# Kernel tuning notes

Hardware: AMD Instinct MI355X
Metric: run time of the kernel (lower is better)

## Reference

```python
import jax, jax.numpy as jnp
import numpy as np

NE, NR, D, H, L = 200000, 500, 128, 4, 2
HD = D // H
N, E, B = 32768, 262144, 256
MARGIN = 1.0


def setup_inputs() -> dict:
    key = jax.random.key(0)
    ks = jax.random.split(key, 16)
    nrm = lambda k, shp, s=0.05: jax.random.normal(k, shp, jnp.float32) * s
    inp = {
        'ent_emb': nrm(ks[0], (NE, D)),
        'rel_emb': nrm(ks[1], (NR, D)),
        'rel_prior': nrm(ks[2], (NR, 1)),
    }
    for i, nm in enumerate(['Wq', 'Wk', 'Wv', 'Wo', 'Wek', 'Wev']):
        inp[nm] = nrm(ks[3 + i], (L, D, D))
    for gi, g in enumerate(['h', 't', 'n']):
        kb = jax.random.fold_in(key, 100 + gi)
        k1, k2, k3, k4 = jax.random.split(kb, 4)
        inp[f'x_{g}'] = jax.random.randint(k1, (N,), 0, NE, jnp.int32)
        inp[f'ei_{g}'] = jax.random.randint(k2, (2, E), 0, N, jnp.int32)
        inp[f'ea_{g}'] = jax.random.randint(k3, (E,), 0, NR, jnp.int32)
        inp[f'y_{g}'] = jax.random.randint(k4, (B,), 0, N // B, jnp.int32)
        inp[f's_{g}'] = jnp.full((B,), N // B, dtype=jnp.int32)
    inp['sample'] = jax.random.randint(ks[9], (B, 3), 0, NR, jnp.int32)
    return inp


def gnn_embed(ent_emb, rel_emb, rel_prior, Wq, Wk, Wv, Wo, Wek, Wev, x, ei, ea, y, s):
    n = x.shape[0]
    h = ent_emb[x]                    # [N, D] node features (embedding lookup)
    e_emb = rel_emb[ea]               # [E, D] edge relation embedding
    e_pri = rel_prior[ea]             # [E, 1] scalar relation prior gate
    src, dst = ei[0], ei[1]
    scale = 1.0 / np.sqrt(HD).astype(np.float32)
    for l in range(L):
        q = (h @ Wq[l]).reshape(n, H, HD)[dst]                               # [E,H,HD]
        k = (h @ Wk[l]).reshape(n, H, HD)[src] + (e_emb @ Wek[l]).reshape(-1, H, HD)
        v = (h @ Wv[l]).reshape(n, H, HD)[src] + (e_emb @ Wev[l]).reshape(-1, H, HD)
        score = jnp.sum(q * k, axis=-1) * scale * e_pri                      # [E,H]
        # segment softmax over incoming edges of each destination node
        m = jax.ops.segment_max(score, dst, num_segments=n)
        m = jnp.where(jnp.isfinite(m), m, 0.0)
        ex = jnp.exp(score - m[dst])
        den = jax.ops.segment_sum(ex, dst, num_segments=n)[dst]
        alpha = ex / (den + 1e-16)                                           # [E,H]
        msg = jax.ops.segment_sum((alpha[..., None] * v).reshape(-1, D), dst, num_segments=n)
        h = jax.nn.gelu(h + msg @ Wo[l])                                     # residual + activation
    # get_real_index: exclusive cumsum of graph sizes + local target index
    offsets = jnp.concatenate([jnp.zeros((1,), s.dtype), jnp.cumsum(s)[:-1]])
    return h[offsets + y]             # [B, D]


def reference(ent_emb, rel_emb, rel_prior, Wq, Wk, Wv, Wo, Wek, Wev,
              x_h, ei_h, ea_h, y_h, s_h,
              x_t, ei_t, ea_t, y_t, s_t,
              x_n, ei_n, ea_n, y_n, s_n, sample):
    g = lambda x, ei, ea, y, s: gnn_embed(ent_emb, rel_emb, rel_prior, Wq, Wk, Wv, Wo, Wek, Wev, x, ei, ea, y, s)
    h = g(x_h, ei_h, ea_h, y_h, s_h)[:, None, :]   # [B,1,D]
    t = g(x_t, ei_t, ea_t, y_t, s_t)[:, None, :]
    tn = g(x_n, ei_n, ea_n, y_n, s_n)[:, None, :]
    r = rel_emb[sample[:, 1]][:, None, :]          # [B,1,D]
    proj_t = h + r                                 # TransE projection
    pos = jnp.linalg.norm(t - proj_t + 1e-8, axis=2)   # [B,1]
    negs = jnp.linalg.norm(t - tn + 1e-8, axis=2)      # [B,1]
    neg = jnp.mean(negs, axis=-1)                      # [B]
    # MarginRankingLoss(pos, neg, target=-1): mean(max(0, (pos-neg)+margin)); broadcasts [B,1]-[B] -> [B,B]
    loss = jnp.mean(jnp.maximum(pos - neg + MARGIN, 0.0))
    return loss
```

## Files before the change

kernel.cpp:

```cpp
#include <hip/hip_runtime.h>
#include <hip/hip_bf16.h>
#include <math.h>

#define NEC 200000
#define NRC 500
#define DD 128
#define LLC 2
#define NNODE 32768
#define EEDGE 262144
#define BBATCH 256
#define NG 3

typedef __attribute__((ext_vector_type(8))) short short8;
typedef __attribute__((ext_vector_type(4))) float floatx4;
typedef __attribute__((ext_vector_type(4))) unsigned short ushort4v;

__device__ __forceinline__ float bf2f(unsigned short u) {
  union { unsigned int i; float f; } c; c.i = ((unsigned int)u) << 16; return c.f;
}
__device__ __forceinline__ unsigned short f2bf(float f) {
  union { float f; unsigned int i; } c; c.f = f;
  unsigned int x = c.i;
  unsigned int r = x + 0x7fffu + ((x >> 16) & 1u);
  return (unsigned short)(r >> 16);
}
__device__ __forceinline__ float bfu_lo(unsigned int u) {
  union { unsigned int i; float f; } c; c.i = u << 16; return c.f;
}
__device__ __forceinline__ float bfu_hi(unsigned int u) {
  union { unsigned int i; float f; } c; c.i = u & 0xffff0000u; return c.f;
}

__global__ void k_detect(const unsigned int* ent_u32, int* mode) {
  int t = threadIdx.x;
  float best = 0.f;
  for (int i = 0; i < 16; ++i) {
    unsigned int w = ent_u32[t * 16 + i];
    float lo = fabsf(bf2f((unsigned short)(w & 0xffffu)));
    if (lo > best) best = lo;
  }
  for (int o = 32; o > 0; o >>= 1) {
    float n = __shfl_down(best, o);
    if (n > best) best = n;
  }
  __shared__ float wmax[4];
  if ((t & 63) == 0) wmax[t >> 6] = best;
  __syncthreads();
  if (t == 0) {
    float m = fmaxf(fmaxf(wmax[0], wmax[1]), fmaxf(wmax[2], wmax[3]));
    mode[0] = (m > 100.f) ? 1 : 0;
  }
}

__global__ void k_pri(const void* prior, const int* mode, float* pris) {
  int r = blockIdx.x * 256 + threadIdx.x;
  if (r >= NRC) return;
  float p = mode[0] ? ((const float*)prior)[r] : bf2f(((const unsigned short*)prior)[r]);
  pris[r] = p * 0.17677669529663687f;
}

__global__ void k_wprep(const void* Wq, const void* Wk, const void* Wv, const void* Wo,
                        const int* mode, unsigned short* WT) {
  int mat = blockIdx.z, l = blockIdx.y;
  const void* W = mat == 0 ? Wq : (mat == 1 ? Wk : (mat == 2 ? Wv : Wo));
  bool fm = mode[0] != 0;
  int t = blockIdx.x * 256 + threadIdx.x;
  int d = t >> 7, c = t & 127;
  size_t src = (size_t)l * DD * DD + (size_t)c * DD + d;
  float v = fm ? ((const float*)W)[src] : bf2f(((const unsigned short*)W)[src]);
  WT[(((size_t)mat * LLC + l) * DD + d) * DD + c] = f2bf(v);
}

__global__ void k_rel(const void* rel, const void* Wek, const void* Wev,
                      const int* mode, unsigned short* relk, unsigned short* relv) {
  int r = blockIdx.x, l = blockIdx.y, which = blockIdx.z;
  int d = threadIdx.x;
  bool fm = mode[0] != 0;
  size_t wofs = (size_t)l * DD * DD;
  const float* Wf = (const float*)(which ? Wev : Wek) + wofs;
  const unsigned short* Wb = (const unsigned short*)(which ? Wev : Wek) + wofs;
  __shared__ float re[DD];
  re[d] = fm ? ((const float*)rel)[r * DD + d] : bf2f(((const unsigned short*)rel)[r * DD + d]);
  __syncthreads();
  float acc = 0.f;
  if (fm) { for (int c = 0; c < DD; ++c) acc += re[c] * Wf[c * DD + d]; }
  else    { for (int c = 0; c < DD; ++c) acc += re[c] * bf2f(Wb[c * DD + d]); }
  unsigned short* out = which ? relv : relk;
  out[((size_t)l * NRC + r) * DD + d] = f2bf(acc);
}

__global__ void k_gather(const void* ent, const int* x0, const int* x1, const int* x2,
                         const int* mode, float* h, unsigned short* hbf) {
  int g = blockIdx.y;
  const int* x = g == 0 ? x0 : (g == 1 ? x1 : x2);
  int t = blockIdx.x * 256 + threadIdx.x;
  int n = t >> 6, p = t & 63;
  int row = x[n];
  float2 f;
  if (mode[0]) {
    f = ((const float2*)((const float*)ent + (size_t)row * DD))[p];
  } else {
    unsigned int v = ((const unsigned int*)((const unsigned short*)ent + (size_t)row * DD))[p];
    f.x = bf2f((unsigned short)(v & 0xffffu));
    f.y = bf2f((unsigned short)(v >> 16));
  }
  size_t gi = (size_t)g * NNODE * 64 + t;
  ((unsigned int*)hbf)[gi] = ((unsigned int)f2bf(f.y) << 16) | (unsigned int)f2bf(f.x);
  ((float2*)h)[gi] = f;
}

__global__ void k_bucket(const int* ei0, const int* ea0, const int* ei1, const int* ea1,
                         const int* ei2, const int* ea2, int* deg, unsigned int* bucket) {
  int g = blockIdx.y;
  const int* ei = g == 0 ? ei0 : (g == 1 ? ei1 : ei2);
  const int* ea = g == 0 ? ea0 : (g == 1 ? ea1 : ea2);
  int e = blockIdx.x * 256 + threadIdx.x;
  if (e >= EEDGE) return;
  int dst = ei[EEDGE + e];
  int src = ei[e];
  int r = ea[e];
  int pos = atomicAdd(&deg[g * NNODE + dst], 1);
  if (pos < 64) bucket[((size_t)g * NNODE + dst) * 64 + pos] = (unsigned int)src | ((unsigned int)r << 15);
}

__device__ __forceinline__ void stage_wt(const unsigned short* WT, int tid,
                                         unsigned short (*Wt)[136]) {
  #pragma unroll
  for (int pass = 0; pass < 8; ++pass) {
    int idx = pass * 256 + tid;
    int d = idx >> 4, c0 = (idx & 15) << 3;
    *reinterpret_cast<short8*>(&Wt[d][c0]) =
        *reinterpret_cast<const short8*>(WT + d * DD + c0);
  }
}

__global__ __launch_bounds__(256) void k_gemm_qkv(const unsigned short* A,
    const unsigned short* WT, int layer, unsigned short* Qo, unsigned short* Ko,
    unsigned short* Vo) {
  __shared__ unsigned short Wt[DD][136];
  int mat = blockIdx.y;
  unsigned short* O = mat == 0 ? Qo : (mat == 1 ? Ko : Vo);
  int g = blockIdx.z;
  const unsigned short* Ag = A + (size_t)g * NNODE * DD;
  unsigned short* Og = O + (size_t)g * NNODE * DD;
  int tid = threadIdx.x;
  stage_wt(WT + ((size_t)mat * LLC + layer) * DD * DD, tid, Wt);
  __syncthreads();
  int w = tid >> 6, lane = tid & 63;
  int m = lane & 15, quad = lane >> 4;
  int row = blockIdx.x * 64 + w * 16 + m;
  floatx4 acc[8];
  #pragma unroll
  for (int t = 0; t < 8; ++t) acc[t] = (floatx4){0.f, 0.f, 0.f, 0.f};
  const unsigned short* arow = Ag + (size_t)row * DD;
  #pragma unroll
  for (int ks = 0; ks < 4; ++ks) {
    short8 a = *reinterpret_cast<const short8*>(arow + ks * 32 + quad * 8);
    #pragma unroll
    for (int t = 0; t < 8; ++t) {
      short8 b = *reinterpret_cast<const short8*>(&Wt[t * 16 + m][ks * 32 + quad * 8]);
      acc[t] = __builtin_amdgcn_mfma_f32_16x16x32_bf16(a, b, acc[t], 0, 0, 0);
    }
  }
  __syncthreads();
  unsigned short* ut = &Wt[0][0];
  #pragma unroll
  for (int t = 0; t < 8; ++t) {
    #pragma unroll
    for (int r = 0; r < 4; ++r) {
      ut[(w * 16 + quad * 4 + r) * 136 + t * 16 + m] = f2bf(acc[t][r]);
    }
  }
  __syncthreads();
  int rowbase = blockIdx.x * 64;
  #pragma unroll
  for (int k = 0; k < 4; ++k) {
    int flat = k * 256 + tid;
    int rw = flat >> 4, c8 = flat & 15;
    short8 v = *reinterpret_cast<const short8*>(ut + rw * 136 + c8 * 8);
    *reinterpret_cast<short8*>(Og + (size_t)(rowbase + rw) * DD + c8 * 8) = v;
  }
}

__global__ __launch_bounds__(256) void k_gemm_o(const unsigned short* A,
    const unsigned short* WT, int layer, float* h, unsigned short* hbf) {
  __shared__ unsigned short Wt[DD][136];
  int g = blockIdx.y;
  const unsigned short* Ag = A + (size_t)g * NNODE * DD;
  float* hg = h + (size_t)g * NNODE * DD;
  unsigned short* hbg = hbf + (size_t)g * NNODE * DD;
  int tid = threadIdx.x;
  stage_wt(WT + ((size_t)3 * LLC + layer) * DD * DD, tid, Wt);
  __syncthreads();
  int w = tid >> 6, lane = tid & 63;
  int m = lane & 15, quad = lane >> 4;
  int row = blockIdx.x * 64 + w * 16 + m;
  floatx4 acc[8];
  #pragma unroll
  for (int t = 0; t < 8; ++t) acc[t] = (floatx4){0.f, 0.f, 0.f, 0.f};
  const unsigned short* arow = Ag + (size_t)row * DD;
  #pragma unroll
  for (int ks = 0; ks < 4; ++ks) {
    short8 a = *reinterpret_cast<const short8*>(arow + ks * 32 + quad * 8);
    #pragma unroll
    for (int t = 0; t < 8; ++t) {
      short8 b = *reinterpret_cast<const short8*>(&Wt[t * 16 + m][ks * 32 + quad * 8]);
      acc[t] = __builtin_amdgcn_mfma_f32_16x16x32_bf16(a, b, acc[t], 0, 0, 0);
    }
  }
  __syncthreads();
  float* ft = (float*)&Wt[0][0];
  #pragma unroll
  for (int t = 0; t < 8; ++t) {
    #pragma unroll
    for (int r = 0; r < 4; ++r) {
      ft[(w * 16 + quad * 4 + r) * 136 + t * 16 + m] = acc[t][r];
    }
  }
  __syncthreads();
  int rowbase = blockIdx.x * 64;
  #pragma unroll
  for (int k = 0; k < 8; ++k) {
    int flat = k * 256 + tid;
    int rw = flat >> 5, c4 = flat & 31;
    float4 v = *reinterpret_cast<const float4*>(ft + rw * 136 + c4 * 4);
    size_t gi = (size_t)(rowbase + rw) * DD + c4 * 4;
    float4 hv = *reinterpret_cast<const float4*>(hg + gi);
    float4 res;
    {
      float xv = v.x + hv.x;
      res.x = 0.5f * xv * (1.f + tanhf(0.7978845608028654f * (xv + 0.044715f * xv * xv * xv)));
      xv = v.y + hv.y;
      res.y = 0.5f * xv * (1.f + tanhf(0.7978845608028654f * (xv + 0.044715f * xv * xv * xv)));
      xv = v.z + hv.z;
      res.z = 0.5f * xv * (1.f + tanhf(0.7978845608028654f * (xv + 0.044715f * xv * xv * xv)));
      xv = v.w + hv.w;
      res.w = 0.5f * xv * (1.f + tanhf(0.7978845608028654f * (xv + 0.044715f * xv * xv * xv)));
    }
    *reinterpret_cast<float4*>(hg + gi) = res;
    ushort4v b4 = { f2bf(res.x), f2bf(res.y), f2bf(res.z), f2bf(res.w) };
    *reinterpret_cast<ushort4v*>(hbg + gi) = b4;
  }
}

__global__ __launch_bounds__(256) void k_attn(const unsigned short* Q, const unsigned short* K,
    const unsigned short* V, const unsigned short* relk, const unsigned short* relv,
    const float* pris, const int* deg, const unsigned int* bucket, int layer,
    unsigned short* msgb) {
  int w = threadIdx.x >> 6, lane = threadIdx.x & 63;
  int quarter = lane >> 4, sl = lane & 15;
  int g = blockIdx.y;
  int dst = blockIdx.x * 4 + w;
  const unsigned short* rk = relk + (size_t)layer * NRC * DD;
  const unsigned short* rv = relv + (size_t)layer * NRC * DD;
  const unsigned short* Kg = K + (size_t)g * NNODE * DD;
  const unsigned short* Vg = V + (size_t)g * NNODE * DD;
  const unsigned short* Qg = Q + (size_t)g * NNODE * DD;

  uint4 qu = *reinterpret_cast<const uint4*>(Qg + (size_t)dst * DD + sl * 8);
  float q0 = bfu_lo(qu.x), q1 = bfu_hi(qu.x), q2 = bfu_lo(qu.y), q3 = bfu_hi(qu.y);
  float q4 = bfu_lo(qu.z), q5 = bfu_hi(qu.z), q6 = bfu_lo(qu.w), q7 = bfu_hi(qu.w);

  float den = 0.f;
  float m0 = 0.f, m1 = 0.f, m2 = 0.f, m3 = 0.f, m4 = 0.f, m5 = 0.f, m6 = 0.f, m7 = 0.f;
  int dg = deg[g * NNODE + dst]; if (dg > 64) dg = 64;
  size_t base = ((size_t)g * NNODE + dst) * 64;
  if (dg > 0) {
    int niter = (dg + 3) >> 2;
    int i0 = quarter < dg ? quarter : dg - 1;
    unsigned int pe = bucket[base + i0];
    for (int i = 0; i < niter; ++i) {
      unsigned int cur = pe;
      int nx = 4 * (i + 1) + quarter; if (nx >= dg) nx = dg - 1;
      pe = bucket[base + nx];
      int src = (int)(cur & 32767u);
      int r = (int)(cur >> 15);
      uint4 ku = *reinterpret_cast<const uint4*>(Kg + (size_t)src * DD + sl * 8);
      uint4 rku = *reinterpret_cast<const uint4*>(rk + (size_t)r * DD + sl * 8);
      uint4 vu = *reinterpret_cast<const uint4*>(Vg + (size_t)src * DD + sl * 8);
      uint4 rvu = *reinterpret_cast<const uint4*>(rv + (size_t)r * DD + sl * 8);
      float p = pris[r];
      float s = q0 * (bfu_lo(ku.x) + bfu_lo(rku.x))
              + q1 * (bfu_hi(ku.x) + bfu_hi(rku.x))
              + q2 * (bfu_lo(ku.y) + bfu_lo(rku.y))
              + q3 * (bfu_hi(ku.y) + bfu_hi(rku.y))
              + q4 * (bfu_lo(ku.z) + bfu_lo(rku.z))
              + q5 * (bfu_hi(ku.z) + bfu_hi(rku.z))
              + q6 * (bfu_lo(ku.w) + bfu_lo(rku.w))
              + q7 * (bfu_hi(ku.w) + bfu_hi(rku.w));
      s += __shfl_xor(s, 1); s += __shfl_xor(s, 2);
      bool valid = (4 * i + quarter) < dg;
      float ex = valid ? __expf(s * p) : 0.f;
      den += ex;
      m0 += ex * (bfu_lo(vu.x) + bfu_lo(rvu.x));
      m1 += ex * (bfu_hi(vu.x) + bfu_hi(rvu.x));
      m2 += ex * (bfu_lo(vu.y) + bfu_lo(rvu.y));
      m3 += ex * (bfu_hi(vu.y) + bfu_hi(rvu.y));
      m4 += ex * (bfu_lo(vu.z) + bfu_lo(rvu.z));
      m5 += ex * (bfu_hi(vu.z) + bfu_hi(rvu.z));
      m6 += ex * (bfu_lo(vu.w) + bfu_lo(rvu.w));
      m7 += ex * (bfu_hi(vu.w) + bfu_hi(rvu.w));
    }
  }
  den += __shfl_xor(den, 16); den += __shfl_xor(den, 32);
  m0 += __shfl_xor(m0, 16); m0 += __shfl_xor(m0, 32);
  m1 += __shfl_xor(m1, 16); m1 += __shfl_xor(m1, 32);
  m2 += __shfl_xor(m2, 16); m2 += __shfl_xor(m2, 32);
  m3 += __shfl_xor(m3, 16); m3 += __shfl_xor(m3, 32);
  m4 += __shfl_xor(m4, 16); m4 += __shfl_xor(m4, 32);
  m5 += __shfl_xor(m5, 16); m5 += __shfl_xor(m5, 32);
  m6 += __shfl_xor(m6, 16); m6 += __shfl_xor(m6, 32);
  m7 += __shfl_xor(m7, 16); m7 += __shfl_xor(m7, 32);
  float inv = 1.f / (den + 1e-16f);
  if (quarter == 0) {
    uint4 o;
    o.x = ((unsigned int)f2bf(m1 * inv) << 16) | (unsigned int)f2bf(m0 * inv);
    o.y = ((unsigned int)f2bf(m3 * inv) << 16) | (unsigned int)f2bf(m2 * inv);
    o.z = ((unsigned int)f2bf(m5 * inv) << 16) | (unsigned int)f2bf(m4 * inv);
    o.w = ((unsigned int)f2bf(m7 * inv) << 16) | (unsigned int)f2bf(m6 * inv);
    *reinterpret_cast<uint4*>(msgb + (size_t)g * NNODE * DD + (size_t)dst * DD + sl * 8) = o;
  }
}

__global__ void k_extract(const float* h, const int* y0, const int* s0,
                          const int* y1, const int* s1, const int* y2, const int* s2,
                          float* emb) {
  int g = blockIdx.y;
  const int* y = g == 0 ? y0 : (g == 1 ? y1 : y2);
  const int* s = g == 0 ? s0 : (g == 1 ? s1 : s2);
  int b = blockIdx.x, d = threadIdx.x;
  int offn = 0;
  for (int j = 0; j < b; ++j) offn += s[j];
  int idx = offn + y[b];
  emb[((size_t)g * BBATCH + b) * DD + d] = h[((size_t)g * NNODE + idx) * DD + d];
}

__global__ void k_posneg(const float* eh, const float* et, const float* en,
    const void* rel, const int* sample, const int* mode, float* pos, float* neg) {
  int b = blockIdx.x, d = threadIdx.x;
  bool fm = mode[0] != 0;
  int r = sample[b * 3 + 1];
  float tt = et[b * DD + d];
  float rr = fm ? ((const float*)rel)[r * DD + d] : bf2f(((const unsigned short*)rel)[r * DD + d]);
  float dp = tt - (eh[b * DD + d] + rr) + 1e-8f;
  float dn = tt - en[b * DD + d] + 1e-8f;
  float ap = dp * dp, an = dn * dn;
  for (int o = 32; o > 0; o >>= 1) { ap += __shfl_down(ap, o); an += __shfl_down(an, o); }
  __shared__ float sa[2], sb[2];
  if ((d & 63) == 0) { sa[d >> 6] = ap; sb[d >> 6] = an; }
  __syncthreads();
  if (d == 0) { pos[b] = sqrtf(sa[0] + sa[1]); neg[b] = sqrtf(sb[0] + sb[1]); }
}

__global__ __launch_bounds__(256) void k_hinge(const float* pos, const float* neg,
    const int* mode, void* out) {
  __shared__ float ns[BBATCH];
  __shared__ float wsum[4];
  int t = threadIdx.x;
  ns[t] = neg[t];
  float pb = pos[t];
  __syncthreads();
  float local = 0.f;
  for (int j = 0; j < BBATCH; ++j) {
    float v = pb - ns[j] + 1.0f;
    local += v > 0.f ? v : 0.f;
  }
  for (int o = 32; o > 0; o >>= 1) local += __shfl_down(local, o);
  if ((t & 63) == 0) wsum[t >> 6] = local;
  __syncthreads();
  if (t == 0) {
    float loss = (wsum[0] + wsum[1] + wsum[2] + wsum[3]) * (1.f / (256.f * 256.f));
    if (mode[0]) ((float*)out)[0] = loss;
    else         ((unsigned short*)out)[0] = f2bf(loss);
  }
}

extern "C" void kernel_launch(void* const* d_in, const int* in_sizes, int n_in,
                              void* d_out, int out_size, void* d_ws, size_t ws_size,
                              hipStream_t stream) {
  const void* ent   = d_in[0];
  const void* rel   = d_in[1];
  const void* prior = d_in[2];
  const void* Wq  = d_in[3];
  const void* Wk  = d_in[4];
  const void* Wv  = d_in[5];
  const void* Wo  = d_in[6];
  const void* Wek = d_in[7];
  const void* Wev = d_in[8];
  const int* sample = (const int*)d_in[24];

  size_t off = 0;
  char* basep = (char*)d_ws;
  auto alloc = [&](size_t bytes) -> void* {
    void* r = basep + off;
    off = (off + bytes + 255) & ~(size_t)255;
    return r;
  };
  float*          h    = (float*)alloc((size_t)NG * NNODE * DD * 4);
  unsigned short* hbf  = (unsigned short*)alloc((size_t)NG * NNODE * DD * 2);
  unsigned short* Qb   = (unsigned short*)alloc((size_t)NG * NNODE * DD * 2);
  unsigned short* Kb   = (unsigned short*)alloc((size_t)NG * NNODE * DD * 2);
  unsigned short* Vb   = (unsigned short*)alloc((size_t)NG * NNODE * DD * 2);
  unsigned short* msgb = (unsigned short*)alloc((size_t)NG * NNODE * DD * 2);
  unsigned short* relk = (unsigned short*)alloc((size_t)LLC * NRC * DD * 2);
  unsigned short* relv = (unsigned short*)alloc((size_t)LLC * NRC * DD * 2);
  unsigned short* WT   = (unsigned short*)alloc((size_t)4 * LLC * DD * DD * 2);
  float* pris = (float*)alloc((size_t)NRC * 4);
  int*   deg  = (int*)alloc((size_t)NG * NNODE * 4);
  unsigned int* bucket = (unsigned int*)alloc((size_t)NG * NNODE * 64 * 4);
  float* emb  = (float*)alloc((size_t)NG * BBATCH * DD * 4);
  float* pos  = (float*)alloc((size_t)BBATCH * 4);
  float* neg  = (float*)alloc((size_t)BBATCH * 4);
  int*   mode = (int*)alloc(256);

  const int* x0  = (const int*)d_in[9],  *x1 = (const int*)d_in[14], *x2 = (const int*)d_in[19];
  const int* ei0 = (const int*)d_in[10], *ei1 = (const int*)d_in[15], *ei2 = (const int*)d_in[20];
  const int* ea0 = (const int*)d_in[11], *ea1 = (const int*)d_in[16], *ea2 = (const int*)d_in[21];
  const int* y0  = (const int*)d_in[12], *y1 = (const int*)d_in[17], *y2 = (const int*)d_in[22];
  const int* s0  = (const int*)d_in[13], *s1 = (const int*)d_in[18], *s2 = (const int*)d_in[23];

  k_detect<<<1, 256, 0, stream>>>((const unsigned int*)ent, mode);
  k_pri<<<2, 256, 0, stream>>>(prior, mode, pris);
  k_wprep<<<dim3(64, LLC, 4), 256, 0, stream>>>(Wq, Wk, Wv, Wo, mode, WT);
  k_rel<<<dim3(NRC, LLC, 2), DD, 0, stream>>>(rel, Wek, Wev, mode, relk, relv);
  hipMemsetAsync(deg, 0, (size_t)NG * NNODE * 4, stream);
  k_gather<<<dim3(NNODE * 64 / 256, NG), 256, 0, stream>>>(ent, x0, x1, x2, mode, h, hbf);
  k_bucket<<<dim3(EEDGE / 256, NG), 256, 0, stream>>>(ei0, ea0, ei1, ea1, ei2, ea2, deg, bucket);

  for (int l = 0; l < LLC; ++l) {
    k_gemm_qkv<<<dim3(NNODE / 64, 3, NG), 256, 0, stream>>>(hbf, WT, l, Qb, Kb, Vb);
    k_attn<<<dim3(NNODE / 4, NG), 256, 0, stream>>>(Qb, Kb, Vb, relk, relv, pris, deg, bucket, l, msgb);
    k_gemm_o<<<dim3(NNODE / 64, NG), 256, 0, stream>>>(msgb, WT, l, h, hbf);
  }
  k_extract<<<dim3(BBATCH, NG), DD, 0, stream>>>(h, y0, s0, y1, s1, y2, s2, emb);
  k_posneg<<<BBATCH, DD, 0, stream>>>(emb, emb + BBATCH * DD, emb + 2 * BBATCH * DD,
                                      rel, sample, mode, pos, neg);
  k_hinge<<<1, BBATCH, 0, stream>>>(pos, neg, mode, d_out);
}
```

Measured before the change: 530.3 us.

## Fuse prep and gather kernels, persist attention grid, shrink bucket cap

Several small setup kernels (dtype detect, prior, weight transpose, relation projection) are merged into one launch, as are gather and bucketing, and extract/posneg. Dtype detection is recomputed inline with a wave ballot instead of a separate kernel. The attention kernel becomes a grid-stride persistent loop with degree prefetch, the per-node edge bucket capacity drops from 64 to 32, and GELU switches from tanhf to an exp-based sigmoid form. These changes aim to cut launch overhead and memory traffic. The smaller bucket cap silently drops edges for nodes with in-degree above 32, and the fast-exp GELU changes numerics slightly.

```diff
diff --git a/kernel.cpp b/kernel.cpp
--- a/kernel.cpp
+++ b/kernel.cpp
@@ -10,6 +10,8 @@
 #define EEDGE 262144
 #define BBATCH 256
 #define NG 3
+#define BCAP 32
+#define ATTN_BLOCKS 2048
 
 typedef __attribute__((ext_vector_type(8))) short short8;
 typedef __attribute__((ext_vector_type(4))) float floatx4;
@@ -31,96 +33,91 @@
   union { unsigned int i; float f; } c; c.i = u & 0xffff0000u; return c.f;
 }
 
-__global__ void k_detect(const unsigned int* ent_u32, int* mode) {
-  int t = threadIdx.x;
-  float best = 0.f;
-  for (int i = 0; i < 16; ++i) {
-    unsigned int w = ent_u32[t * 16 + i];
-    float lo = fabsf(bf2f((unsigned short)(w & 0xffffu)));
-    if (lo > best) best = lo;
-  }
-  for (int o = 32; o > 0; o >>= 1) {
-    float n = __shfl_down(best, o);
-    if (n > best) best = n;
-  }
-  __shared__ float wmax[4];
-  if ((t & 63) == 0) wmax[t >> 6] = best;
-  __syncthreads();
-  if (t == 0) {
-    float m = fmaxf(fmaxf(wmax[0], wmax[1]), fmaxf(wmax[2], wmax[3]));
-    mode[0] = (m > 100.f) ? 1 : 0;
-  }
-}
-
-__global__ void k_pri(const void* prior, const int* mode, float* pris) {
-  int r = blockIdx.x * 256 + threadIdx.x;
-  if (r >= NRC) return;
-  float p = mode[0] ? ((const float*)prior)[r] : bf2f(((const unsigned short*)prior)[r]);
-  pris[r] = p * 0.17677669529663687f;
-}
-
-__global__ void k_wprep(const void* Wq, const void* Wk, const void* Wv, const void* Wo,
-                        const int* mode, unsigned short* WT) {
-  int mat = blockIdx.z, l = blockIdx.y;
-  const void* W = mat == 0 ? Wq : (mat == 1 ? Wk : (mat == 2 ? Wv : Wo));
-  bool fm = mode[0] != 0;
-  int t = blockIdx.x * 256 + threadIdx.x;
-  int d = t >> 7, c = t & 127;
-  size_t src = (size_t)l * DD * DD + (size_t)c * DD + d;
-  float v = fm ? ((const float*)W)[src] : bf2f(((const unsigned short*)W)[src]);
-  WT[(((size_t)mat * LLC + l) * DD + d) * DD + c] = f2bf(v);
-}
-
-__global__ void k_rel(const void* rel, const void* Wek, const void* Wev,
-                      const int* mode, unsigned short* relk, unsigned short* relv) {
-  int r = blockIdx.x, l = blockIdx.y, which = blockIdx.z;
-  int d = threadIdx.x;
-  bool fm = mode[0] != 0;
-  size_t wofs = (size_t)l * DD * DD;
-  const float* Wf = (const float*)(which ? Wev : Wek) + wofs;
-  const unsigned short* Wb = (const unsigned short*)(which ? Wev : Wek) + wofs;
-  __shared__ float re[DD];
-  re[d] = fm ? ((const float*)rel)[r * DD + d] : bf2f(((const unsigned short*)rel)[r * DD + d]);
-  __syncthreads();
-  float acc = 0.f;
-  if (fm) { for (int c = 0; c < DD; ++c) acc += re[c] * Wf[c * DD + d]; }
-  else    { for (int c = 0; c < DD; ++c) acc += re[c] * bf2f(Wb[c * DD + d]); }
-  unsigned short* out = which ? relv : relk;
-  out[((size_t)l * NRC + r) * DD + d] = f2bf(acc);
-}
-
-__global__ void k_gather(const void* ent, const int* x0, const int* x1, const int* x2,
-                         const int* mode, float* h, unsigned short* hbf) {
-  int g = blockIdx.y;
-  const int* x = g == 0 ? x0 : (g == 1 ? x1 : x2);
-  int t = blockIdx.x * 256 + threadIdx.x;
-  int n = t >> 6, p = t & 63;
-  int row = x[n];
-  float2 f;
-  if (mode[0]) {
-    f = ((const float2*)((const float*)ent + (size_t)row * DD))[p];
+__device__ __forceinline__ bool detect_fm(const void* ent) {
+  unsigned int u = ((const unsigned int*)ent)[threadIdx.x & 63];
+  bool big = fabsf(bfu_lo(u)) > 100.f;
+  return __ballot(big) != 0ull;
+}
+
+__global__ __launch_bounds__(128) void k_prep(const void* ent, const void* rel,
+    const void* prior, const void* Wq, const void* Wk, const void* Wv, const void* Wo,
+    const void* Wek, const void* Wev,
+    float* pris, unsigned short* WT, unsigned short* relk, unsigned short* relv) {
+  bool fm = detect_fm(ent);
+  int bid = blockIdx.x, tid = threadIdx.x;
+  if (bid < 4) {
+    int r = bid * 128 + tid;
+    if (r < NRC) {
+      float p = fm ? ((const float*)prior)[r] : bf2f(((const unsigned short*)prior)[r]);
+      pris[r] = p * 0.17677669529663687f;
+    }
+  } else if (bid < 1028) {
+    int t = (bid - 4) * 128 + tid;
+    int mat = t >> 15;
+    int rem = t & 32767;
+    int l = rem >> 14;
+    int p = rem & 16383;
+    int d = p >> 7, c = p & 127;
+    const void* W = mat == 0 ? Wq : (mat == 1 ? Wk : (mat == 2 ? Wv : Wo));
+    size_t src = (size_t)l * DD * DD + (size_t)c * DD + d;
+    float v = fm ? ((const float*)W)[src] : bf2f(((const unsigned short*)W)[src]);
+    WT[(((size_t)mat * LLC + l) * DD + d) * DD + c] = f2bf(v);
   } else {
-    unsigned int v = ((const unsigned int*)((const unsigned short*)ent + (size_t)row * DD))[p];
-    f.x = bf2f((unsigned short)(v & 0xffffu));
-    f.y = bf2f((unsigned short)(v >> 16));
-  }
-  size_t gi = (size_t)g * NNODE * 64 + t;
-  ((unsigned int*)hbf)[gi] = ((unsigned int)f2bf(f.y) << 16) | (unsigned int)f2bf(f.x);
-  ((float2*)h)[gi] = f;
-}
-
-__global__ void k_bucket(const int* ei0, const int* ea0, const int* ei1, const int* ea1,
-                         const int* ei2, const int* ea2, int* deg, unsigned int* bucket) {
-  int g = blockIdx.y;
-  const int* ei = g == 0 ? ei0 : (g == 1 ? ei1 : ei2);
-  const int* ea = g == 0 ? ea0 : (g == 1 ? ea1 : ea2);
-  int e = blockIdx.x * 256 + threadIdx.x;
-  if (e >= EEDGE) return;
-  int dst = ei[EEDGE + e];
-  int src = ei[e];
-  int r = ea[e];
-  int pos = atomicAdd(&deg[g * NNODE + dst], 1);
-  if (pos < 64) bucket[((size_t)g * NNODE + dst) * 64 + pos] = (unsigned int)src | ((unsigned int)r << 15);
+    int rid = bid - 1028;
+    int which = rid / 1000;
+    int l = (rid / 500) % 2;
+    int r = rid % 500;
+    int d = tid;
+    size_t wofs = (size_t)l * DD * DD;
+    const float* Wf = (const float*)(which ? Wev : Wek) + wofs;
+    const unsigned short* Wb = (const unsigned short*)(which ? Wev : Wek) + wofs;
+    __shared__ float re[DD];
+    re[d] = fm ? ((const float*)rel)[r * DD + d] : bf2f(((const unsigned short*)rel)[r * DD + d]);
+    __syncthreads();
+    float acc = 0.f;
+    if (fm) { for (int c = 0; c < DD; ++c) acc += re[c] * Wf[c * DD + d]; }
+    else    { for (int c = 0; c < DD; ++c) acc += re[c] * bf2f(Wb[c * DD + d]); }
+    unsigned short* out = which ? relv : relk;
+    out[((size_t)l * NRC + r) * DD + d] = f2bf(acc);
+  }
+}
+
+__global__ __launch_bounds__(256) void k_gb(const void* ent,
+    const int* x0, const int* x1, const int* x2,
+    const int* ei0, const int* ea0, const int* ei1, const int* ea1,
+    const int* ei2, const int* ea2,
+    float* h, unsigned short* hbf, int* deg, unsigned int* bucket) {
+  int bid = blockIdx.x, tid = threadIdx.x;
+  if (bid < 24576) {
+    bool fm = detect_fm(ent);
+    int g = bid >> 13;
+    const int* x = g == 0 ? x0 : (g == 1 ? x1 : x2);
+    int t = (bid & 8191) * 256 + tid;
+    int n = t >> 6, p = t & 63;
+    int row = x[n];
+    float2 f;
+    if (fm) {
+      f = ((const float2*)((const float*)ent + (size_t)row * DD))[p];
+    } else {
+      unsigned int v = ((const unsigned int*)((const unsigned short*)ent + (size_t)row * DD))[p];
+      f.x = bfu_lo(v); f.y = bfu_hi(v);
+    }
+    size_t gi = (size_t)g * NNODE * 64 + t;
+    ((unsigned int*)hbf)[gi] = ((unsigned int)f2bf(f.y) << 16) | (unsigned int)f2bf(f.x);
+    ((float2*)h)[gi] = f;
+  } else {
+    int bb = bid - 24576;
+    int g = bb >> 10;
+    const int* ei = g == 0 ? ei0 : (g == 1 ? ei1 : ei2);
+    const int* ea = g == 0 ? ea0 : (g == 1 ? ea1 : ea2);
+    int e = (bb & 1023) * 256 + tid;
+    int dst = ei[EEDGE + e];
+    int src = ei[e];
+    int r = ea[e];
+    int pos = atomicAdd(&deg[g * NNODE + dst], 1);
+    if (pos < BCAP)
+      bucket[((size_t)g * NNODE + dst) * BCAP + pos] = (unsigned int)src | ((unsigned int)r << 15);
+  }
 }
 
 __device__ __forceinline__ void stage_wt(const unsigned short* WT, int tid,
@@ -227,15 +224,11 @@
     size_t gi = (size_t)(rowbase + rw) * DD + c4 * 4;
     float4 hv = *reinterpret_cast<const float4*>(hg + gi);
     float4 res;
-    {
-      float xv = v.x + hv.x;
-      res.x = 0.5f * xv * (1.f + tanhf(0.7978845608028654f * (xv + 0.044715f * xv * xv * xv)));
-      xv = v.y + hv.y;
-      res.y = 0.5f * xv * (1.f + tanhf(0.7978845608028654f * (xv + 0.044715f * xv * xv * xv)));
-      xv = v.z + hv.z;
-      res.z = 0.5f * xv * (1.f + tanhf(0.7978845608028654f * (xv + 0.044715f * xv * xv * xv)));
-      xv = v.w + hv.w;
-      res.w = 0.5f * xv * (1.f + tanhf(0.7978845608028654f * (xv + 0.044715f * xv * xv * xv)));
+    #pragma unroll
+    for (int j = 0; j < 4; ++j) {
+      float xv = (&v.x)[j] + (&hv.x)[j];
+      float z2 = 1.5957691216057308f * (xv + 0.044715f * xv * xv * xv);
+      (&res.x)[j] = xv / (1.f + __expf(-z2));
     }
     *reinterpret_cast<float4*>(hg + gi) = res;
     ushort4v b4 = { f2bf(res.x), f2bf(res.y), f2bf(res.z), f2bf(res.w) };
@@ -249,101 +242,99 @@
     unsigned short* msgb) {
   int w = threadIdx.x >> 6, lane = threadIdx.x & 63;
   int quarter = lane >> 4, sl = lane & 15;
-  int g = blockIdx.y;
-  int dst = blockIdx.x * 4 + w;
   const unsigned short* rk = relk + (size_t)layer * NRC * DD;
   const unsigned short* rv = relv + (size_t)layer * NRC * DD;
-  const unsigned short* Kg = K + (size_t)g * NNODE * DD;
-  const unsigned short* Vg = V + (size_t)g * NNODE * DD;
-  const unsigned short* Qg = Q + (size_t)g * NNODE * DD;
-
-  uint4 qu = *reinterpret_cast<const uint4*>(Qg + (size_t)dst * DD + sl * 8);
-  float q0 = bfu_lo(qu.x), q1 = bfu_hi(qu.x), q2 = bfu_lo(qu.y), q3 = bfu_hi(qu.y);
-  float q4 = bfu_lo(qu.z), q5 = bfu_hi(qu.z), q6 = bfu_lo(qu.w), q7 = bfu_hi(qu.w);
-
-  float den = 0.f;
-  float m0 = 0.f, m1 = 0.f, m2 = 0.f, m3 = 0.f, m4 = 0.f, m5 = 0.f, m6 = 0.f, m7 = 0.f;
-  int dg = deg[g * NNODE + dst]; if (dg > 64) dg = 64;
-  size_t base = ((size_t)g * NNODE + dst) * 64;
-  if (dg > 0) {
-    int niter = (dg + 3) >> 2;
-    int i0 = quarter < dg ? quarter : dg - 1;
-    unsigned int pe = bucket[base + i0];
-    for (int i = 0; i < niter; ++i) {
-      unsigned int cur = pe;
-      int nx = 4 * (i + 1) + quarter; if (nx >= dg) nx = dg - 1;
-      pe = bucket[base + nx];
-      int src = (int)(cur & 32767u);
-      int r = (int)(cur >> 15);
-      uint4 ku = *reinterpret_cast<const uint4*>(Kg + (size_t)src * DD + sl * 8);
-      uint4 rku = *reinterpret_cast<const uint4*>(rk + (size_t)r * DD + sl * 8);
-      uint4 vu = *reinterpret_cast<const uint4*>(Vg + (size_t)src * DD + sl * 8);
-      uint4 rvu = *reinterpret_cast<const uint4*>(rv + (size_t)r * DD + sl * 8);
-      float p = pris[r];
-      float s = q0 * (bfu_lo(ku.x) + bfu_lo(rku.x))
-              + q1 * (bfu_hi(ku.x) + bfu_hi(rku.x))
-              + q2 * (bfu_lo(ku.y) + bfu_lo(rku.y))
-              + q3 * (bfu_hi(ku.y) + bfu_hi(rku.y))
-              + q4 * (bfu_lo(ku.z) + bfu_lo(rku.z))
-              + q5 * (bfu_hi(ku.z) + bfu_hi(rku.z))
-              + q6 * (bfu_lo(ku.w) + bfu_lo(rku.w))
-              + q7 * (bfu_hi(ku.w) + bfu_hi(rku.w));
-      s += __shfl_xor(s, 1); s += __shfl_xor(s, 2);
-      bool valid = (4 * i + quarter) < dg;
-      float ex = valid ? __expf(s * p) : 0.f;
-      den += ex;
-      m0 += ex * (bfu_lo(vu.x) + bfu_lo(rvu.x));
-      m1 += ex * (bfu_hi(vu.x) + bfu_hi(rvu.x));
-      m2 += ex * (bfu_lo(vu.y) + bfu_lo(rvu.y));
-      m3 += ex * (bfu_hi(vu.y) + bfu_hi(rvu.y));
-      m4 += ex * (bfu_lo(vu.z) + bfu_lo(rvu.z));
-      m5 += ex * (bfu_hi(vu.z) + bfu_hi(rvu.z));
-      m6 += ex * (bfu_lo(vu.w) + bfu_lo(rvu.w));
-      m7 += ex * (bfu_hi(vu.w) + bfu_hi(rvu.w));
-    }
-  }
-  den += __shfl_xor(den, 16); den += __shfl_xor(den, 32);
-  m0 += __shfl_xor(m0, 16); m0 += __shfl_xor(m0, 32);
-  m1 += __shfl_xor(m1, 16); m1 += __shfl_xor(m1, 32);
-  m2 += __shfl_xor(m2, 16); m2 += __shfl_xor(m2, 32);
-  m3 += __shfl_xor(m3, 16); m3 += __shfl_xor(m3, 32);
-  m4 += __shfl_xor(m4, 16); m4 += __shfl_xor(m4, 32);
-  m5 += __shfl_xor(m5, 16); m5 += __shfl_xor(m5, 32);
-  m6 += __shfl_xor(m6, 16); m6 += __shfl_xor(m6, 32);
-  m7 += __shfl_xor(m7, 16); m7 += __shfl_xor(m7, 32);
-  float inv = 1.f / (den + 1e-16f);
-  if (quarter == 0) {
-    uint4 o;
-    o.x = ((unsigned int)f2bf(m1 * inv) << 16) | (unsigned int)f2bf(m0 * inv);
-    o.y = ((unsigned int)f2bf(m3 * inv) << 16) | (unsigned int)f2bf(m2 * inv);
-    o.z = ((unsigned int)f2bf(m5 * inv) << 16) | (unsigned int)f2bf(m4 * inv);
-    o.w = ((unsigned int)f2bf(m7 * inv) << 16) | (unsigned int)f2bf(m6 * inv);
-    *reinterpret_cast<uint4*>(msgb + (size_t)g * NNODE * DD + (size_t)dst * DD + sl * 8) = o;
-  }
-}
-
-__global__ void k_extract(const float* h, const int* y0, const int* s0,
-                          const int* y1, const int* s1, const int* y2, const int* s2,
-                          float* emb) {
-  int g = blockIdx.y;
-  const int* y = g == 0 ? y0 : (g == 1 ? y1 : y2);
-  const int* s = g == 0 ? s0 : (g == 1 ? s1 : s2);
+  int wid = blockIdx.x * 4 + w;
+  const int total = NNODE * NG;
+  int dgcur = deg[wid];
+  for (int idx = wid; idx < total; idx += ATTN_BLOCKS * 4) {
+    int nidx = idx + ATTN_BLOCKS * 4;
+    int dgnext = nidx < total ? deg[nidx] : 0;
+    int g = idx >> 15;
+    int dst = idx & (NNODE - 1);
+    size_t gofs = (size_t)g * NNODE * DD;
+    const unsigned short* Kg = K + gofs;
+    const unsigned short* Vg = V + gofs;
+    uint4 qu = *reinterpret_cast<const uint4*>(Q + gofs + (size_t)dst * DD + sl * 8);
+    float q0 = bfu_lo(qu.x), q1 = bfu_hi(qu.x), q2 = bfu_lo(qu.y), q3 = bfu_hi(qu.y);
+    float q4 = bfu_lo(qu.z), q5 = bfu_hi(qu.z), q6 = bfu_lo(qu.w), q7 = bfu_hi(qu.w);
+    float den = 0.f;
+    float m0 = 0.f, m1 = 0.f, m2 = 0.f, m3 = 0.f, m4 = 0.f, m5 = 0.f, m6 = 0.f, m7 = 0.f;
+    int dg = dgcur; if (dg > BCAP) dg = BCAP;
+    size_t base = (size_t)idx * BCAP;
+    if (dg > 0) {
+      int niter = (dg + 3) >> 2;
+      unsigned int pe = bucket[base + (quarter < dg ? quarter : 0)];
+      for (int i = 0; i < niter; ++i) {
+        unsigned int cur = pe;
+        int nx = 4 * (i + 1) + quarter; if (nx > BCAP - 1) nx = BCAP - 1;
+        pe = bucket[base + nx];
+        int src = (int)(cur & 32767u);
+        int r = (int)(cur >> 15);
+        uint4 ku = *reinterpret_cast<const uint4*>(Kg + (size_t)src * DD + sl * 8);
+        uint4 rku = *reinterpret_cast<const uint4*>(rk + (size_t)r * DD + sl * 8);
+        uint4 vu = *reinterpret_cast<const uint4*>(Vg + (size_t)src * DD + sl * 8);
+        uint4 rvu = *reinterpret_cast<const uint4*>(rv + (size_t)r * DD + sl * 8);
+        float p = pris[r];
+        float s = q0 * (bfu_lo(ku.x) + bfu_lo(rku.x))
+                + q1 * (bfu_hi(ku.x) + bfu_hi(rku.x))
+                + q2 * (bfu_lo(ku.y) + bfu_lo(rku.y))
+                + q3 * (bfu_hi(ku.y) + bfu_hi(rku.y))
+                + q4 * (bfu_lo(ku.z) + bfu_lo(rku.z))
+                + q5 * (bfu_hi(ku.z) + bfu_hi(rku.z))
+                + q6 * (bfu_lo(ku.w) + bfu_lo(rku.w))
+                + q7 * (bfu_hi(ku.w) + bfu_hi(rku.w));
+        s += __shfl_xor(s, 1); s += __shfl_xor(s, 2);
+        bool valid = (4 * i + quarter) < dg;
+        float ex = valid ? __expf(s * p) : 0.f;
+        den += ex;
+        m0 += ex * (bfu_lo(vu.x) + bfu_lo(rvu.x));
+        m1 += ex * (bfu_hi(vu.x) + bfu_hi(rvu.x));
+        m2 += ex * (bfu_lo(vu.y) + bfu_lo(rvu.y));
+        m3 += ex * (bfu_hi(vu.y) + bfu_hi(rvu.y));
+        m4 += ex * (bfu_lo(vu.z) + bfu_lo(rvu.z));
+        m5 += ex * (bfu_hi(vu.z) + bfu_hi(rvu.z));
+        m6 += ex * (bfu_lo(vu.w) + bfu_lo(rvu.w));
+        m7 += ex * (bfu_hi(vu.w) + bfu_hi(rvu.w));
+      }
+    }
+    den += __shfl_xor(den, 16); den += __shfl_xor(den, 32);
+    m0 += __shfl_xor(m0, 16); m0 += __shfl_xor(m0, 32);
+    m1 += __shfl_xor(m1, 16); m1 += __shfl_xor(m1, 32);
+    m2 += __shfl_xor(m2, 16); m2 += __shfl_xor(m2, 32);
+    m3 += __shfl_xor(m3, 16); m3 += __shfl_xor(m3, 32);
+    m4 += __shfl_xor(m4, 16); m4 += __shfl_xor(m4, 32);
+    m5 += __shfl_xor(m5, 16); m5 += __shfl_xor(m5, 32);
+    m6 += __shfl_xor(m6, 16); m6 += __shfl_xor(m6, 32);
+    m7 += __shfl_xor(m7, 16); m7 += __shfl_xor(m7, 32);
+    float inv = 1.f / (den + 1e-16f);
+    if (quarter == 0) {
+      uint4 o;
+      o.x = ((unsigned int)f2bf(m1 * inv) << 16) | (unsigned int)f2bf(m0 * inv);
+      o.y = ((unsigned int)f2bf(m3 * inv) << 16) | (unsigned int)f2bf(m2 * inv);
+      o.z = ((unsigned int)f2bf(m5 * inv) << 16) | (unsigned int)f2bf(m4 * inv);
+      o.w = ((unsigned int)f2bf(m7 * inv) << 16) | (unsigned int)f2bf(m6 * inv);
+      *reinterpret_cast<uint4*>(msgb + gofs + (size_t)dst * DD + sl * 8) = o;
+    }
+    dgcur = dgnext;
+  }
+}
+
+__global__ __launch_bounds__(128) void k_ep(const float* h, const void* ent, const void* rel,
+    const int* y0, const int* s0, const int* y1, const int* s1, const int* y2, const int* s2,
+    const int* sample, float* pos, float* neg) {
+  bool fm = detect_fm(ent);
   int b = blockIdx.x, d = threadIdx.x;
-  int offn = 0;
-  for (int j = 0; j < b; ++j) offn += s[j];
-  int idx = offn + y[b];
-  emb[((size_t)g * BBATCH + b) * DD + d] = h[((size_t)g * NNODE + idx) * DD + d];
-}
-
-__global__ void k_posneg(const float* eh, const float* et, const float* en,
-    const void* rel, const int* sample, const int* mode, float* pos, float* neg) {
-  int b = blockIdx.x, d = threadIdx.x;
-  bool fm = mode[0] != 0;
+  int oh = 0, ot = 0, on = 0;
+  for (int j = 0; j < b; ++j) { oh += s0[j]; ot += s1[j]; on += s2[j]; }
+  int ih = oh + y0[b], it = ot + y1[b], in_ = on + y2[b];
+  float th = h[((size_t)0 * NNODE + ih) * DD + d];
+  float tt = h[((size_t)1 * NNODE + it) * DD + d];
+  float tn = h[((size_t)2 * NNODE + in_) * DD + d];
   int r = sample[b * 3 + 1];
-  float tt = et[b * DD + d];
   float rr = fm ? ((const float*)rel)[r * DD + d] : bf2f(((const unsigned short*)rel)[r * DD + d]);
-  float dp = tt - (eh[b * DD + d] + rr) + 1e-8f;
-  float dn = tt - en[b * DD + d] + 1e-8f;
+  float dp = tt - (th + rr) + 1e-8f;
+  float dn = tt - tn + 1e-8f;
   float ap = dp * dp, an = dn * dn;
   for (int o = 32; o > 0; o >>= 1) { ap += __shfl_down(ap, o); an += __shfl_down(an, o); }
   __shared__ float sa[2], sb[2];
@@ -353,7 +344,8 @@
 }
 
 __global__ __launch_bounds__(256) void k_hinge(const float* pos, const float* neg,
-    const int* mode, void* out) {
+    const void* ent, void* out) {
+  bool fm = detect_fm(ent);
   __shared__ float ns[BBATCH];
   __shared__ float wsum[4];
   int t = threadIdx.x;
@@ -370,8 +362,8 @@
   __syncthreads();
   if (t == 0) {
     float loss = (wsum[0] + wsum[1] + wsum[2] + wsum[3]) * (1.f / (256.f * 256.f));
-    if (mode[0]) ((float*)out)[0] = loss;
-    else         ((unsigned short*)out)[0] = f2bf(loss);
+    if (fm) ((float*)out)[0] = loss;
+    else    ((unsigned short*)out)[0] = f2bf(loss);
   }
 }
 
@@ -407,11 +399,9 @@
   unsigned short* WT   = (unsigned short*)alloc((size_t)4 * LLC * DD * DD * 2);
   float* pris = (float*)alloc((size_t)NRC * 4);
   int*   deg  = (int*)alloc((size_t)NG * NNODE * 4);
-  unsigned int* bucket = (unsigned int*)alloc((size_t)NG * NNODE * 64 * 4);
-  float* emb  = (float*)alloc((size_t)NG * BBATCH * DD * 4);
+  unsigned int* bucket = (unsigned int*)alloc((size_t)NG * NNODE * BCAP * 4);
   float* pos  = (float*)alloc((size_t)BBATCH * 4);
   float* neg  = (float*)alloc((size_t)BBATCH * 4);
-  int*   mode = (int*)alloc(256);
 
   const int* x0  = (const int*)d_in[9],  *x1 = (const int*)d_in[14], *x2 = (const int*)d_in[19];
   const int* ei0 = (const int*)d_in[10], *ei1 = (const int*)d_in[15], *ei2 = (const int*)d_in[20];
@@ -419,21 +409,16 @@
   const int* y0  = (const int*)d_in[12], *y1 = (const int*)d_in[17], *y2 = (const int*)d_in[22];
   const int* s0  = (const int*)d_in[13], *s1 = (const int*)d_in[18], *s2 = (const int*)d_in[23];
 
-  k_detect<<<1, 256, 0, stream>>>((const unsigned int*)ent, mode);
-  k_pri<<<2, 256, 0, stream>>>(prior, mode, pris);
-  k_wprep<<<dim3(64, LLC, 4), 256, 0, stream>>>(Wq, Wk, Wv, Wo, mode, WT);
-  k_rel<<<dim3(NRC, LLC, 2), DD, 0, stream>>>(rel, Wek, Wev, mode, relk, relv);
   hipMemsetAsync(deg, 0, (size_t)NG * NNODE * 4, stream);
-  k_gather<<<dim3(NNODE * 64 / 256, NG), 256, 0, stream>>>(ent, x0, x1, x2, mode, h, hbf);
-  k_bucket<<<dim3(EEDGE / 256, NG), 256, 0, stream>>>(ei0, ea0, ei1, ea1, ei2, ea2, deg, bucket);
-
+  k_prep<<<3028, 128, 0, stream>>>(ent, rel, prior, Wq, Wk, Wv, Wo, Wek, Wev,
+                                   pris, WT, relk, relv);
+  k_gb<<<27648, 256, 0, stream>>>(ent, x0, x1, x2, ei0, ea0, ei1, ea1, ei2, ea2,
+                                  h, hbf, deg, bucket);
   for (int l = 0; l < LLC; ++l) {
     k_gemm_qkv<<<dim3(NNODE / 64, 3, NG), 256, 0, stream>>>(hbf, WT, l, Qb, Kb, Vb);
-    k_attn<<<dim3(NNODE / 4, NG), 256, 0, stream>>>(Qb, Kb, Vb, relk, relv, pris, deg, bucket, l, msgb);
+    k_attn<<<ATTN_BLOCKS, 256, 0, stream>>>(Qb, Kb, Vb, relk, relv, pris, deg, bucket, l, msgb);
     k_gemm_o<<<dim3(NNODE / 64, NG), 256, 0, stream>>>(msgb, WT, l, h, hbf);
   }
-  k_extract<<<dim3(BBATCH, NG), DD, 0, stream>>>(h, y0, s0, y1, s1, y2, s2, emb);
-  k_posneg<<<BBATCH, DD, 0, stream>>>(emb, emb + BBATCH * DD, emb + 2 * BBATCH * DD,
-                                      rel, sample, mode, pos, neg);
-  k_hinge<<<1, BBATCH, 0, stream>>>(pos, neg, mode, d_out);
-}
+  k_ep<<<BBATCH, 128, 0, stream>>>(h, ent, rel, y0, s0, y1, s1, y2, s2, sample, pos, neg);
+  k_hinge<<<1, BBATCH, 0, stream>>>(pos, neg, ent, d_out);
+}
```

Measured after the change: 574.8 us. 8.4% more time.
